# Optimization experiments

Measured on AMD Instinct MI355X. Metric: run time of the kernel, lower is better.

Reference implementation:

```python
import jax, jax.numpy as jnp
import numpy as np
import math

PSIZE = [(8, 8), (16, 16)]


def _conv2d(x, w, b):
    # 3x3 stride-1 'SAME' conv, NCHW / OIHW
    y = jax.lax.conv_general_dilated(
        x, w, window_strides=(1, 1), padding='SAME',
        dimension_numbers=('NCHW', 'OIHW', 'NCHW'))
    return y + b[None, :, None, None]


def _patch_attention(x, xs, b, t, c, h, w, ph, pw):
    oh, ow = h // ph, w // pw
    d = c * ph * pw
    # query: [b, oh*ow, c*ph*pw]
    q = x.reshape(b, c, oh, ph, ow, pw).transpose(0, 2, 4, 1, 3, 5).reshape(b, oh * ow, d)
    # key/value: [b, t*oh*ow, c*ph*pw]
    k = xs.reshape(b, t, c, oh, ph, ow, pw).transpose(0, 1, 3, 5, 2, 4, 6).reshape(b, t * oh * ow, d)
    scores = jnp.einsum('bqd,bkd->bqk', q, k) / jnp.asarray(math.sqrt(d), x.dtype)
    # NOTE: the original torch code calls scores.masked_fill(mm, -1e9) without
    # assigning the result, so the mask has NO effect; we faithfully omit it.
    atten = jax.nn.softmax(scores, axis=-1)
    val = jnp.einsum('bqk,bkd->bqd', atten, k)
    y = val.reshape(b, oh, ow, c, ph, pw).transpose(0, 3, 1, 4, 2, 5).reshape(b, c, h, w)
    return y


def setup_inputs() -> dict:
    key = jax.random.key(0)
    ks = jax.random.split(key, 6)
    b, t, c, h, w = 2, 5, 256, 128, 128
    n_p = len(PSIZE)
    x = jax.random.normal(ks[0], (b, c, h, w), dtype=jnp.float32)
    xs = jax.random.normal(ks[1], (b * t, c, h, w), dtype=jnp.float32)
    ms = jax.random.uniform(ks[2], (b * t, 1, h, w), dtype=jnp.float32)
    fan_lin = c * n_p * 9
    w_lin = jax.random.normal(ks[3], (c, c * n_p, 3, 3), dtype=jnp.float32) * (1.0 / math.sqrt(fan_lin))
    b_lin = jnp.zeros((c,), dtype=jnp.float32)
    fan_g = 512 * 9
    w_gate = jax.random.normal(ks[4], (c, 2 * c, 3, 3), dtype=jnp.float32) * (1.0 / math.sqrt(fan_g))
    b_gate = jnp.zeros((c,), dtype=jnp.float32)
    w_feat = jax.random.normal(ks[5], (c, 2 * c, 3, 3), dtype=jnp.float32) * (1.0 / math.sqrt(fan_g))
    b_feat = jnp.zeros((c,), dtype=jnp.float32)
    return {'x': x, 'xs': xs, 'ms': ms, 'w_lin': w_lin, 'b_lin': b_lin,
            'w_gate': w_gate, 'b_gate': b_gate, 'w_feat': w_feat, 'b_feat': b_feat}


def reference(x, xs, ms, w_lin, b_lin, w_gate, b_gate, w_feat, b_feat):
    b, c, h, w = x.shape
    t = xs.shape[0] // b
    outs = [_patch_attention(x, xs, b, t, c, h, w, ph, pw) for (ph, pw) in PSIZE]
    out = jnp.concatenate(outs, axis=1)                    # [b, c*len(psize), h, w]
    out = jax.nn.leaky_relu(_conv2d(out, w_lin, b_lin), 0.2)  # [b, c, h, w]
    fused = jnp.concatenate([x, out], axis=1)              # [b, 2c, h, w]
    gating = _conv2d(fused, w_gate, b_gate)
    feature = jax.nn.leaky_relu(_conv2d(fused, w_feat, b_feat), 0.2)
    x_out = jax.nn.sigmoid(gating) * feature               # [b, c, h, w]
    return x_out
```

## Files before the change

### kernel.cpp

```cpp
#include <hip/hip_runtime.h>

typedef unsigned short u16;
typedef unsigned int u32;
typedef __attribute__((ext_vector_type(8))) short bf16x8;
typedef __attribute__((ext_vector_type(4))) float f32x4;

#define MFMA16(d, a, bb) d = __builtin_amdgcn_mfma_f32_16x16x32_bf16(a, bb, d, 0, 0, 0)

#define PROW 130
#define PIMG 16900
#define PIMGC (16900 * 512)

__device__ __forceinline__ u16 f2bf(float f){
  union { float f; u32 i; } v; v.f = f;
  u32 r = v.i + 0x7fffu + ((v.i >> 16) & 1u);
  return (u16)(r >> 16);
}

__device__ __forceinline__ void gl16(const u16* g, u16* l){
  __builtin_amdgcn_global_load_lds(
      (const __attribute__((address_space(1))) u32*)g,
      (__attribute__((address_space(3))) u32*)l, 16, 0, 0);
}

__global__ __launch_bounds__(256) void k_border(u16* __restrict__ buf){
  const int b = blockIdx.y;
  const int j = blockIdx.x * 4 + (threadIdx.x >> 6);
  const int l = threadIdx.x & 63;
  int pp;
  if(j < 130)       pp = j;
  else if(j < 260)  pp = 129 * 130 + (j - 130);
  else if(j < 388)  pp = (j - 259) * 130;
  else              pp = (j - 387) * 130 + 129;
  u16* p = buf + ((size_t)b * PIMG + pp) * 512 + l * 8;
  *(uint4*)p = (uint4){0u, 0u, 0u, 0u};
}

__global__ __launch_bounds__(256) void k_transpose_pad(const float* __restrict__ in,
                                                       u16* __restrict__ out){
  __shared__ float s[32][33];
  const float* ip = in + (size_t)blockIdx.z * 256 * 16384;
  u16* op = out + (size_t)blockIdx.z * PIMGC;
  int r0 = blockIdx.x * 32, c0 = blockIdx.y * 32;
  int tx = threadIdx.x, ty = threadIdx.y;
#pragma unroll
  for(int i = 0; i < 4; ++i){
    int r = ty * 4 + i;
    s[r][tx] = ip[(size_t)(r0 + r) * 16384 + (c0 + tx)];
  }
  __syncthreads();
#pragma unroll
  for(int i = 0; i < 4; ++i){
    int pix = c0 + ty * 4 + i;
    u32 pp = ((u32)(pix >> 7) + 1) * PROW + (pix & 127) + 1;
    op[(size_t)pp * 512 + (r0 + tx)] = f2bf(s[tx][ty * 4 + i]);
  }
}

__global__ __launch_bounds__(256) void k_transpose(const float* __restrict__ in,
                                                   u16* __restrict__ out,
                                                   int rows, int cols,
                                                   int ostride, size_t o_imgstride){
  __shared__ float s[32][33];
  const float* ip = in + (size_t)blockIdx.z * (size_t)rows * (size_t)cols;
  u16* op = out + (size_t)blockIdx.z * o_imgstride;
  int r0 = blockIdx.x * 32, c0 = blockIdx.y * 32;
  int tx = threadIdx.x, ty = threadIdx.y;
#pragma unroll
  for(int i = 0; i < 4; ++i){
    int r = ty * 4 + i;
    s[r][tx] = ip[(size_t)(r0 + r) * cols + (c0 + tx)];
  }
  __syncthreads();
#pragma unroll
  for(int i = 0; i < 4; ++i){
    int c = ty * 4 + i;
    op[(size_t)(c0 + c) * ostride + (r0 + tx)] = f2bf(s[tx][c]);
  }
}

__global__ __launch_bounds__(256) void k_wt(const float* __restrict__ in,
                                            u16* __restrict__ out,
                                            int co_mul, int co_off, int co_tot){
  int ci = blockIdx.x * 256 + threadIdx.x;
  int co = blockIdx.y;
  int e  = blockIdx.z;
  out[((size_t)e * co_tot + co * co_mul + co_off) * 512 + ci] =
      f2bf(in[((size_t)co * 512 + ci) * 9 + e]);
}

__global__ __launch_bounds__(256) void k_scores8(const u16* __restrict__ FUSEDP,
                                                 const u16* __restrict__ XST,
                                                 float* __restrict__ S8p){
  __shared__ u16 As[4096], Bs[4096];
  const int bz = blockIdx.z, b = bz >> 3, g = bz & 7;
  const int q0 = blockIdx.x * 128, k0 = blockIdx.y * 128;
  const int tid = threadIdx.x, w = tid >> 6, l = tid & 63;
  const int wr = w >> 1, wc = w & 1;
  const int l15 = l & 15, kg = (l >> 4) * 8;
  f32x4 acc[4][4];
#pragma unroll
  for(int m = 0; m < 4; ++m)
#pragma unroll
    for(int n = 0; n < 4; ++n) acc[m][n] = (f32x4){0.f, 0.f, 0.f, 0.f};

  for(int e8 = 0; e8 < 8; ++e8){
    const int e = g * 8 + e8, dy = e >> 3, dx = e & 7;
    for(int ci0 = 0; ci0 < 256; ci0 += 32){
#pragma unroll
      for(int r = 0; r < 2; ++r){
        const int idx = (w * 2 + r) * 64 + l;
        const int q = q0 + (idx >> 2);
        const int apy = ((q >> 4) << 3) + dy, apx = ((q & 15) << 3) + dx;
        const size_t pa = ((size_t)b * PIMG + (size_t)(apy + 1) * PROW + apx + 1) * 512
                          + ci0 + (idx & 3) * 8;
        gl16(FUSEDP + pa, As + (size_t)(w * 2 + r) * 512);
        const int k = k0 + (idx >> 2), t = k >> 8, rm = k & 255;
        const size_t pb = (((size_t)b * 5 + t) * 16384 +
                           (size_t)(((rm >> 4) << 3) + dy) * 128 + ((rm & 15) << 3) + dx) * 256
                          + ci0 + (idx & 3) * 8;
        gl16(XST + pb, Bs + (size_t)(w * 2 + r) * 512);
      }
      __syncthreads();
      bf16x8 af[4], bq[4];
#pragma unroll
      for(int m = 0; m < 4; ++m) af[m] = *(const bf16x8*)(As + (wr * 64 + m * 16 + l15) * 32 + kg);
#pragma unroll
      for(int n = 0; n < 4; ++n) bq[n] = *(const bf16x8*)(Bs + (wc * 64 + n * 16 + l15) * 32 + kg);
#pragma unroll
      for(int m = 0; m < 4; ++m)
#pragma unroll
        for(int n = 0; n < 4; ++n)
          acc[m][n] = __builtin_amdgcn_mfma_f32_16x16x32_bf16(af[m], bq[n], acc[m][n], 0, 0, 0);
      __syncthreads();
    }
  }
  float* dst = S8p + ((size_t)g * 2 + b) * 256 * 1280;
#pragma unroll
  for(int m = 0; m < 4; ++m){
    const int q = q0 + wr * 64 + m * 16 + (l >> 4) * 4;
#pragma unroll
    for(int n = 0; n < 4; ++n){
      const int k = k0 + wc * 64 + n * 16 + l15;
#pragma unroll
      for(int r = 0; r < 4; ++r) dst[(size_t)(q + r) * 1280 + k] = acc[m][n][r];
    }
  }
}

__global__ __launch_bounds__(256) void k_softmax8(const float* __restrict__ S8p,
                                                  u16* __restrict__ A8){
  __shared__ float red[8];
  int b = blockIdx.x >> 8, q = blockIdx.x & 255;
  size_t roff = ((size_t)b * 256 + q) * 1280;
  int tid = threadIdx.x;
  float v[5]; float m = -1e30f;
#pragma unroll
  for(int i = 0; i < 5; ++i){
    size_t o = roff + tid + 256 * i;
    float s = 0.f;
#pragma unroll
    for(int g = 0; g < 8; ++g) s += S8p[(size_t)g * 655360 + o];
    v[i] = s * 0.0078125f; m = fmaxf(m, v[i]);
  }
#pragma unroll
  for(int o = 32; o > 0; o >>= 1) m = fmaxf(m, __shfl_xor(m, o));
  int wid = tid >> 6;
  if((tid & 63) == 0) red[wid] = m;
  __syncthreads();
  m = fmaxf(fmaxf(red[0], red[1]), fmaxf(red[2], red[3]));
  float s = 0.f;
#pragma unroll
  for(int i = 0; i < 5; ++i){ v[i] = __expf(v[i] - m); s += v[i]; }
#pragma unroll
  for(int o = 32; o > 0; o >>= 1) s += __shfl_xor(s, o);
  if((tid & 63) == 0) red[4 + wid] = s;
  __syncthreads();
  s = red[4] + red[5] + red[6] + red[7];
  float inv = 1.0f / s;
#pragma unroll
  for(int i = 0; i < 5; ++i) A8[roff + tid + 256 * i] = f2bf(v[i] * inv);
}

__global__ __launch_bounds__(320) void k_s16(const float* __restrict__ S8p,
                                             u16* __restrict__ A16){
  __shared__ float red[10];
  int b = blockIdx.x >> 6, q16 = blockIdx.x & 63;
  int tid = threadIdx.x;
  int t = tid >> 6, rm = tid & 63;
  int KY = rm >> 3, KX = rm & 7;
  int QY = q16 >> 3, QX = q16 & 7;
  float s = 0.f;
#pragma unroll
  for(int i = 0; i < 2; ++i)
#pragma unroll
    for(int j = 0; j < 2; ++j){
      int q8 = (2 * QY + i) * 16 + (2 * QX + j);
      int k8 = t * 256 + (2 * KY + i) * 16 + (2 * KX + j);
      size_t o = ((size_t)b * 256 + q8) * 1280 + k8;
#pragma unroll
      for(int g = 0; g < 8; ++g) s += S8p[(size_t)g * 655360 + o];
    }
  s *= 0.00390625f;
  float m = s;
#pragma unroll
  for(int o = 32; o > 0; o >>= 1) m = fmaxf(m, __shfl_xor(m, o));
  int wid = tid >> 6;
  if((tid & 63) == 0) red[wid] = m;
  __syncthreads();
  m = fmaxf(fmaxf(fmaxf(red[0], red[1]), fmaxf(red[2], red[3])), red[4]);
  float e = __expf(s - m);
  float sm = e;
#pragma unroll
  for(int o = 32; o > 0; o >>= 1) sm += __shfl_xor(sm, o);
  if((tid & 63) == 0) red[5 + wid] = sm;
  __syncthreads();
  sm = red[5] + red[6] + red[7] + red[8] + red[9];
  A16[((size_t)b * 64 + q16) * 320 + tid] = f2bf(e / sm);
}

__global__ __launch_bounds__(256) void k_val8(const u16* __restrict__ A8,
                                              const u16* __restrict__ XST,
                                              u16* __restrict__ OUTCATP){
  __shared__ u16 As[4096];
  __shared__ u16 Bs[128 * 40];
  const int z = blockIdx.z, b = z >> 6, rr = z & 63;
  const int ry = rr >> 3, rx = rr & 7;
  const int q0 = blockIdx.x * 128, c0 = blockIdx.y * 128;
  const int tid = threadIdx.x, w = tid >> 6, l = tid & 63;
  const int wr = w >> 1, wc = w & 1;
  const int l15 = l & 15, kg = (l >> 4) * 8;
  const int k2 = tid >> 4, ch8 = tid & 15;
  f32x4 acc[4][4];
#pragma unroll
  for(int m = 0; m < 4; ++m)
#pragma unroll
    for(int n = 0; n < 4; ++n) acc[m][n] = (f32x4){0.f, 0.f, 0.f, 0.f};

  for(int k0 = 0; k0 < 1280; k0 += 32){
#pragma unroll
    for(int r = 0; r < 2; ++r){
      const int idx = (w * 2 + r) * 64 + l;
      const u16* ga = A8 + ((size_t)b * 256 + q0 + (idx >> 2)) * 1280 + k0 + (idx & 3) * 8;
      gl16(ga, As + (size_t)(w * 2 + r) * 512);
    }
    {
      const int ka = k0 + k2 * 2, kb = ka + 1;
      const int ta = ka >> 8, ra = ka & 255;
      const int tb = kb >> 8, rb = kb & 255;
      const size_t pa = (((size_t)b * 5 + ta) * 16384 +
                         (size_t)(((ra >> 4) << 3) + ry) * 128 + ((ra & 15) << 3) + rx) * 256
                        + c0 + ch8 * 8;
      const size_t pb = (((size_t)b * 5 + tb) * 16384 +
                         (size_t)(((rb >> 4) << 3) + ry) * 128 + ((rb & 15) << 3) + rx) * 256
                        + c0 + ch8 * 8;
      union { uint4 v; u16 s[8]; } u0, u1;
      u0.v = *(const uint4*)(XST + pa);
      u1.v = *(const uint4*)(XST + pb);
      const int kloc = k2 * 2, swz = (ch8 & 3) << 3;
#pragma unroll
      for(int j = 0; j < 8; ++j){
        u32 pack = (u32)u0.s[j] | ((u32)u1.s[j] << 16);
        *(u32*)(Bs + (size_t)(ch8 * 8 + j) * 40 + (kloc ^ swz)) = pack;
      }
    }
    __syncthreads();
    bf16x8 af[4], bq[4];
#pragma unroll
    for(int m = 0; m < 4; ++m) af[m] = *(const bf16x8*)(As + (wr * 64 + m * 16 + l15) * 32 + kg);
#pragma unroll
    for(int n = 0; n < 4; ++n){
      const int ch = wc * 64 + n * 16 + l15;
      bq[n] = *(const bf16x8*)(Bs + (size_t)ch * 40 + (kg ^ (((ch >> 3) & 3) << 3)));
    }
#pragma unroll
    for(int m = 0; m < 4; ++m)
#pragma unroll
      for(int n = 0; n < 4; ++n)
        acc[m][n] = __builtin_amdgcn_mfma_f32_16x16x32_bf16(af[m], bq[n], acc[m][n], 0, 0, 0);
    __syncthreads();
  }
#pragma unroll
  for(int m = 0; m < 4; ++m){
    const int qb = q0 + wr * 64 + m * 16 + (l >> 4) * 4;
#pragma unroll
    for(int n = 0; n < 4; ++n){
      const int ch = c0 + wc * 64 + n * 16 + l15;
#pragma unroll
      for(int r = 0; r < 4; ++r){
        const int q = qb + r;
        const int py = ((q >> 4) << 3) + ry, px = ((q & 15) << 3) + rx;
        OUTCATP[((size_t)b * PIMG + (size_t)(py + 1) * PROW + px + 1) * 512 + ch] = f2bf(acc[m][n][r]);
      }
    }
  }
}

__global__ __launch_bounds__(256) void k_val16(const u16* __restrict__ A16,
                                               const u16* __restrict__ XST,
                                               u16* __restrict__ OUTCATP){
  __shared__ u16 As[64 * 32];
  __shared__ u16 Bs[128 * 40];
  const int z = blockIdx.z, b = z >> 8, rr = z & 255;
  const int ry = rr >> 4, rx = rr & 15;
  const int c0 = blockIdx.y * 128;
  const int tid = threadIdx.x, w = tid >> 6, l = tid & 63;
  const int l15 = l & 15, kg = (l >> 4) * 8;
  const int k2 = tid >> 4, ch8 = tid & 15;
  f32x4 acc[4][2];
#pragma unroll
  for(int m = 0; m < 4; ++m)
#pragma unroll
    for(int n = 0; n < 2; ++n) acc[m][n] = (f32x4){0.f, 0.f, 0.f, 0.f};

  for(int k0 = 0; k0 < 320; k0 += 32){
    {
      const int idx = w * 64 + l;
      const u16* ga = A16 + ((size_t)b * 64 + (idx >> 2)) * 320 + k0 + (idx & 3) * 8;
      gl16(ga, As + (size_t)w * 512);
    }
    {
      const int ka = k0 + k2 * 2, kb = ka + 1;
      const int ta = ka >> 6, ra = ka & 63;
      const int tb = kb >> 6, rb = kb & 63;
      const size_t pa = (((size_t)b * 5 + ta) * 16384 +
                         (size_t)(((ra >> 3) << 4) + ry) * 128 + ((ra & 7) << 4) + rx) * 256
                        + c0 + ch8 * 8;
      const size_t pb = (((size_t)b * 5 + tb) * 16384 +
                         (size_t)(((rb >> 3) << 4) + ry) * 128 + ((rb & 7) << 4) + rx) * 256
                        + c0 + ch8 * 8;
      union { uint4 v; u16 s[8]; } u0, u1;
      u0.v = *(const uint4*)(XST + pa);
      u1.v = *(const uint4*)(XST + pb);
      const int kloc = k2 * 2, swz = (ch8 & 3) << 3;
#pragma unroll
      for(int j = 0; j < 8; ++j){
        u32 pack = (u32)u0.s[j] | ((u32)u1.s[j] << 16);
        *(u32*)(Bs + (size_t)(ch8 * 8 + j) * 40 + (kloc ^ swz)) = pack;
      }
    }
    __syncthreads();
    bf16x8 af[4], bq[2];
#pragma unroll
    for(int m = 0; m < 4; ++m) af[m] = *(const bf16x8*)(As + (m * 16 + l15) * 32 + kg);
#pragma unroll
    for(int n = 0; n < 2; ++n){
      const int ch = w * 32 + n * 16 + l15;
      bq[n] = *(const bf16x8*)(Bs + (size_t)ch * 40 + (kg ^ (((ch >> 3) & 3) << 3)));
    }
#pragma unroll
    for(int m = 0; m < 4; ++m)
#pragma unroll
      for(int n = 0; n < 2; ++n)
        acc[m][n] = __builtin_amdgcn_mfma_f32_16x16x32_bf16(af[m], bq[n], acc[m][n], 0, 0, 0);
    __syncthreads();
  }
#pragma unroll
  for(int m = 0; m < 4; ++m){
    const int qb = m * 16 + (l >> 4) * 4;
#pragma unroll
    for(int n = 0; n < 2; ++n){
      const int ch = c0 + w * 32 + n * 16 + l15;
#pragma unroll
      for(int r = 0; r < 4; ++r){
        const int q = qb + r;
        const int py = ((q >> 3) << 4) + ry, px = ((q & 7) << 4) + rx;
        OUTCATP[((size_t)b * PIMG + (size_t)(py + 1) * PROW + px + 1) * 512 + 256 + ch] = f2bf(acc[m][n][r]);
      }
    }
  }
}

__global__ __launch_bounds__(512, 4) void k_convA(const u16* __restrict__ A,
                                                  const u16* __restrict__ W,
                                                  const float* __restrict__ bias,
                                                  u16* __restrict__ FUSEDP){
  constexpr int NT = 72;
  __shared__ u16 lds[2][16384];
  const int id = blockIdx.x;
  const int wg = (id & 7) * 64 + (id >> 3);
  const int mt = wg & 127, rest = wg >> 7;
  const int n0 = (rest & 1) * 128, b = rest >> 1;
  const int m0 = mt * 128;
  const int tid = threadIdx.x, w = tid >> 6, l = tid & 63;
  const int wr = w >> 2, wc = w & 3;
  const int l15 = l & 15, lq = l >> 4;
  const int lr = l >> 3;
  const u32 laneswz = (u32)((((l & 7) * 16) ^ (lr << 4)) >> 1);

  u32 aB[2], bB[2];
#pragma unroll
  for(int j = 0; j < 2; ++j){
    const int row = (w * 2 + j) * 8 + lr;
    const int p = m0 + row;
    aB[j] = ((u32)b * PIMG + ((u32)(p >> 7) + 1) * PROW + (u32)(p & 127) + 1) * 512 + laneswz;
    bB[j] = (u32)(n0 + row) * 512 + laneswz;
  }

  f32x4 acc[4][2];
#pragma unroll
  for(int m = 0; m < 4; ++m)
#pragma unroll
    for(int n = 0; n < 2; ++n) acc[m][n] = (f32x4){0.f, 0.f, 0.f, 0.f};

  auto STAGE = [&](int kt){
    const int e = kt % 9, ci0 = (kt / 9) << 6;
    const int dy = e / 3 - 1, dx = e % 3 - 1;
    const int aD = (dy * PROW + dx) * 512 + ci0;
    const u32 bD = (u32)e * 256u * 512u + ci0;
    u16* bufA = &lds[kt & 1][0];
    u16* bufB = &lds[kt & 1][8192];
#pragma unroll
    for(int j = 0; j < 2; ++j){
      const int c = w * 2 + j;
      gl16(A + aB[j] + aD, bufA + c * 512);
      gl16(W + bB[j] + bD, bufB + c * 512);
    }
  };

  STAGE(0);
  STAGE(1);

  for(int t = 0; t < NT; ++t){
    if(t < NT - 1) asm volatile("s_waitcnt vmcnt(4)" ::: "memory");
    else           asm volatile("s_waitcnt vmcnt(0)" ::: "memory");
    __builtin_amdgcn_s_barrier();
    const char* bufA = (const char*)&lds[t & 1][0];
    const char* bufB = bufA + 16384;
    bf16x8 af[4][2], bq[2][2];
#pragma unroll
    for(int m = 0; m < 4; ++m){
      const int row = wr * 64 + m * 16 + l15;
      const int sz = (row & 7) << 4;
#pragma unroll
      for(int kk = 0; kk < 2; ++kk)
        af[m][kk] = *(const bf16x8*)(bufA + row * 128 + (((kk * 4 + lq) * 16) ^ sz));
    }
#pragma unroll
    for(int n = 0; n < 2; ++n){
      const int row = wc * 32 + n * 16 + l15;
      const int sz = (row & 7) << 4;
#pragma unroll
      for(int kk = 0; kk < 2; ++kk)
        bq[n][kk] = *(const bf16x8*)(bufB + row * 128 + (((kk * 4 + lq) * 16) ^ sz));
    }
    asm volatile("s_waitcnt lgkmcnt(0)" ::: "memory");
    __builtin_amdgcn_sched_barrier(0);
    __builtin_amdgcn_s_barrier();
    if(t + 2 < NT) STAGE(t + 2);
    __builtin_amdgcn_s_setprio(1);
#pragma unroll
    for(int kk = 0; kk < 2; ++kk)
#pragma unroll
      for(int m = 0; m < 4; ++m)
#pragma unroll
        for(int n = 0; n < 2; ++n)
          MFMA16(acc[m][n], af[m][kk], bq[n][kk]);
    __builtin_amdgcn_s_setprio(0);
  }

#pragma unroll
  for(int m = 0; m < 4; ++m){
    const int p0 = m0 + wr * 64 + m * 16 + lq * 4;
    const size_t pp = ((size_t)b * PIMG + (size_t)((p0 >> 7) + 1) * PROW + (p0 & 127) + 1) * 512;
#pragma unroll
    for(int n = 0; n < 2; ++n){
      const int co = n0 + wc * 32 + n * 16 + l15;
      const float bi = bias[co];
#pragma unroll
      for(int r = 0; r < 4; ++r){
        float v = acc[m][n][r] + bi;
        v = v > 0.f ? v : 0.2f * v;
        FUSEDP[pp + (size_t)r * 512 + 256 + co] = f2bf(v);
      }
    }
  }
}

__global__ __launch_bounds__(1024, 4) void k_convB16(const u16* __restrict__ A,
                                                     const u16* __restrict__ W,
                                                     const float* __restrict__ bias,
                                                     const float* __restrict__ bias2,
                                                     float* __restrict__ out){
  constexpr int NT = 72;
  __shared__ u16 lds[2][32768];
  const int id = blockIdx.x;
  const int wg = (id & 7) * 32 + (id >> 3);
  const int ntile = wg >> 7;
  const int rem = wg & 127, b = rem >> 6, mt = rem & 63;
  const int m0 = mt * 256, n0 = ntile * 256;
  const int tid = threadIdx.x, w = tid >> 6, l = tid & 63;
  const int wr = w >> 2, wc = w & 3;
  const int l15 = l & 15, lq = l >> 4;
  const int lr = l >> 3;
  const u32 laneswz = (u32)((((l & 7) * 16) ^ (lr << 4)) >> 1);

  u32 aB[2], bB[2];
#pragma unroll
  for(int j = 0; j < 2; ++j){
    const int row = (w * 2 + j) * 8 + lr;
    const int p = m0 + row;
    aB[j] = ((u32)b * PIMG + ((u32)(p >> 7) + 1) * PROW + (u32)(p & 127) + 1) * 512 + laneswz;
    bB[j] = (u32)(n0 + row) * 512 + laneswz;
  }

  f32x4 acc[4][4];
#pragma unroll
  for(int m = 0; m < 4; ++m)
#pragma unroll
    for(int n = 0; n < 4; ++n) acc[m][n] = (f32x4){0.f, 0.f, 0.f, 0.f};

  auto STAGE = [&](int kt){
    const int e = kt % 9, ci0 = (kt / 9) << 6;
    const int dy = e / 3 - 1, dx = e % 3 - 1;
    const int aD = (dy * PROW + dx) * 512 + ci0;
    const u32 bD = (u32)e * 512u * 512u + ci0;
    u16* bufA = &lds[kt & 1][0];
    u16* bufB = &lds[kt & 1][16384];
#pragma unroll
    for(int j = 0; j < 2; ++j){
      const int c = w * 2 + j;
      gl16(A + aB[j] + aD, bufA + c * 512);
      gl16(W + bB[j] + bD, bufB + c * 512);
    }
  };

  STAGE(0);
  STAGE(1);

  for(int t = 0; t < NT; ++t){
    if(t < NT - 1) asm volatile("s_waitcnt vmcnt(4)" ::: "memory");
    else           asm volatile("s_waitcnt vmcnt(0)" ::: "memory");
    __builtin_amdgcn_s_barrier();
    const char* bufA = (const char*)&lds[t & 1][0];
    const char* bufB = bufA + 32768;
    bf16x8 af[4], bq[4];
#pragma unroll
    for(int m = 0; m < 4; ++m){
      const int row = wr * 64 + m * 16 + l15;
      af[m] = *(const bf16x8*)(bufA + row * 128 + ((lq * 16) ^ ((row & 7) << 4)));
    }
#pragma unroll
    for(int n = 0; n < 4; ++n){
      const int row = wc * 64 + n * 16 + l15;
      bq[n] = *(const bf16x8*)(bufB + row * 128 + ((lq * 16) ^ ((row & 7) << 4)));
    }
    asm volatile("s_waitcnt lgkmcnt(0)" ::: "memory");
    __builtin_amdgcn_sched_barrier(0);
    __builtin_amdgcn_s_setprio(1);
#pragma unroll
    for(int m = 0; m < 4; ++m)
#pragma unroll
      for(int n = 0; n < 4; ++n)
        MFMA16(acc[m][n], af[m], bq[n]);
    __builtin_amdgcn_s_setprio(0);
#pragma unroll
    for(int m = 0; m < 4; ++m){
      const int row = wr * 64 + m * 16 + l15;
      af[m] = *(const bf16x8*)(bufA + row * 128 + ((64 + lq * 16) ^ ((row & 7) << 4)));
    }
#pragma unroll
    for(int n = 0; n < 4; ++n){
      const int row = wc * 64 + n * 16 + l15;
      bq[n] = *(const bf16x8*)(bufB + row * 128 + ((64 + lq * 16) ^ ((row & 7) << 4)));
    }
    asm volatile("s_waitcnt lgkmcnt(0)" ::: "memory");
    __builtin_amdgcn_sched_barrier(0);
    __builtin_amdgcn_s_barrier();
    if(t + 2 < NT) STAGE(t + 2);
    __builtin_amdgcn_s_setprio(1);
#pragma unroll
    for(int m = 0; m < 4; ++m)
#pragma unroll
      for(int n = 0; n < 4; ++n)
        MFMA16(acc[m][n], af[m], bq[n]);
    __builtin_amdgcn_s_setprio(0);
  }

#pragma unroll
  for(int m = 0; m < 4; ++m){
    const int p0 = m0 + wr * 64 + m * 16 + lq * 4;
#pragma unroll
    for(int n = 0; n < 4; ++n){
      const int col = n0 + wc * 64 + n * 16 + l15;
      const int s = col & 1, co = col >> 1;
      const float big = bias[co], bif = bias2[co];
      float res[4];
#pragma unroll
      for(int r = 0; r < 4; ++r){
        const float val = acc[m][n][r];
        const float oth = __shfl_xor(val, 1);
        float gg = s ? oth : val;
        float ff = s ? val : oth;
        gg += big; ff += bif;
        ff = ff > 0.f ? ff : 0.2f * ff;
        res[r] = ff / (1.0f + __expf(-gg));
      }
      if(s == 0){
        float4 v4 = make_float4(res[0], res[1], res[2], res[3]);
        *(float4*)&out[((size_t)b * 256 + co) * 16384 + p0] = v4;
      }
    }
  }
}

extern "C" void kernel_launch(void* const* d_in, const int* in_sizes, int n_in,
                              void* d_out, int out_size, void* d_ws, size_t ws_size,
                              hipStream_t stream){
  const float* x      = (const float*)d_in[0];
  const float* xs     = (const float*)d_in[1];
  const float* w_lin  = (const float*)d_in[3];
  const float* b_lin  = (const float*)d_in[4];
  const float* w_gate = (const float*)d_in[5];
  const float* b_gate = (const float*)d_in[6];
  const float* w_feat = (const float*)d_in[7];
  const float* b_feat = (const float*)d_in[8];
  float* out = (float*)d_out;

  char* ws = (char*)d_ws;
  size_t off = 0;
  auto alloc = [&](size_t bytes) -> void* {
    void* p = ws + off;
    off += (bytes + 255) & ~(size_t)255;
    return p;
  };
  u16* FUSEDP  = (u16*)alloc(2ull * PIMGC * 2);
  u16* OUTCATP = (u16*)alloc(2ull * PIMGC * 2);
  u16* XST     = (u16*)alloc(10ull * 16384 * 256 * 2);
  u16* WTl     = (u16*)alloc(9ull * 256 * 512 * 2);
  u16* WGF     = (u16*)alloc(9ull * 512 * 512 * 2);
  float* S8p   = (float*)alloc(8ull * 655360 * 4);
  u16* A8      = (u16*)alloc(655360ull * 2);
  u16* A16     = (u16*)alloc(2ull * 64 * 320 * 2);

  k_border<<<dim3(129, 2), 256, 0, stream>>>(FUSEDP);
  k_border<<<dim3(129, 2), 256, 0, stream>>>(OUTCATP);

  dim3 tb(32, 8);
  k_transpose_pad<<<dim3(8, 512, 2), tb, 0, stream>>>(x, FUSEDP);
  k_transpose<<<dim3(8, 512, 10), tb, 0, stream>>>(xs, XST, 256, 16384, 256, 4194304ull);

  k_wt<<<dim3(2, 256, 9), 256, 0, stream>>>(w_lin,  WTl, 1, 0, 256);
  k_wt<<<dim3(2, 256, 9), 256, 0, stream>>>(w_gate, WGF, 2, 0, 512);
  k_wt<<<dim3(2, 256, 9), 256, 0, stream>>>(w_feat, WGF, 2, 1, 512);

  k_scores8<<<dim3(2, 10, 16), 256, 0, stream>>>(FUSEDP, XST, S8p);
  k_softmax8<<<512, 256, 0, stream>>>(S8p, A8);
  k_s16<<<128, 320, 0, stream>>>(S8p, A16);

  k_val8 <<<dim3(2, 2, 128), 256, 0, stream>>>(A8, XST, OUTCATP);
  k_val16<<<dim3(1, 2, 512), 256, 0, stream>>>(A16, XST, OUTCATP);

  k_convA<<<512, 512, 0, stream>>>(OUTCATP, WTl, b_lin, FUSEDP);
  k_convB16<<<256, 1024, 0, stream>>>(FUSEDP, WGF, b_gate, b_feat, out);
}
```

Before: 405.2 us.

## Vectorize transposes, coalesce weight reorder, double-buffer swizzled scores8 GEMM

Transpose kernels now handle 64-channel tiles and emit 16-byte packed bf16 stores instead of scalar u16 writes. Weight reordering reads each input's 9 taps contiguously in one thread rather than striding. The 8x8 score GEMM moves to 512 threads with double-buffered LDS, 64-wide K steps, an XOR-swizzled LDS layout, explicit waitcnt/barrier pipelining and raised MFMA priority, all aimed at hiding global-load latency and avoiding LDS bank conflicts. This adds fragile hand-written vmcnt counts and much more LDS per block.

```diff
diff --git a/kernel.cpp b/kernel.cpp
--- a/kernel.cpp
+++ b/kernel.cpp
@@ -36,112 +36,159 @@
   *(uint4*)p = (uint4){0u, 0u, 0u, 0u};
 }
 
-__global__ __launch_bounds__(256) void k_transpose_pad(const float* __restrict__ in,
-                                                       u16* __restrict__ out){
-  __shared__ float s[32][33];
+__global__ __launch_bounds__(256) void k_transPadW(const float* __restrict__ in,
+                                                   u16* __restrict__ out){
+  __shared__ float s[64][33];
   const float* ip = in + (size_t)blockIdx.z * 256 * 16384;
   u16* op = out + (size_t)blockIdx.z * PIMGC;
-  int r0 = blockIdx.x * 32, c0 = blockIdx.y * 32;
-  int tx = threadIdx.x, ty = threadIdx.y;
-#pragma unroll
-  for(int i = 0; i < 4; ++i){
-    int r = ty * 4 + i;
+  const int r0 = blockIdx.x * 64, c0 = blockIdx.y * 32;
+  const int tx = threadIdx.x, ty = threadIdx.y;
+#pragma unroll
+  for(int i = 0; i < 8; ++i){
+    int r = ty * 8 + i;
     s[r][tx] = ip[(size_t)(r0 + r) * 16384 + (c0 + tx)];
   }
   __syncthreads();
-#pragma unroll
-  for(int i = 0; i < 4; ++i){
-    int pix = c0 + ty * 4 + i;
-    u32 pp = ((u32)(pix >> 7) + 1) * PROW + (pix & 127) + 1;
-    op[(size_t)pp * 512 + (r0 + tx)] = f2bf(s[tx][ty * 4 + i]);
-  }
-}
-
-__global__ __launch_bounds__(256) void k_transpose(const float* __restrict__ in,
-                                                   u16* __restrict__ out,
-                                                   int rows, int cols,
-                                                   int ostride, size_t o_imgstride){
-  __shared__ float s[32][33];
-  const float* ip = in + (size_t)blockIdx.z * (size_t)rows * (size_t)cols;
+  const int tid = ty * 32 + tx;
+  const int p = tid >> 3, cs = (tid & 7) * 8;
+  const int pix = c0 + p;
+  const u32 pp = ((u32)(pix >> 7) + 1) * PROW + (pix & 127) + 1;
+  union { uint4 v; u16 h[8]; } pk;
+#pragma unroll
+  for(int i = 0; i < 8; ++i) pk.h[i] = f2bf(s[cs + i][p]);
+  *(uint4*)(op + (size_t)pp * 512 + r0 + cs) = pk.v;
+}
+
+__global__ __launch_bounds__(256) void k_transW(const float* __restrict__ in,
+                                                u16* __restrict__ out,
+                                                int cols, int ostride,
+                                                size_t o_imgstride){
+  __shared__ float s[64][33];
+  const float* ip = in + (size_t)blockIdx.z * 256 * (size_t)cols;
   u16* op = out + (size_t)blockIdx.z * o_imgstride;
-  int r0 = blockIdx.x * 32, c0 = blockIdx.y * 32;
-  int tx = threadIdx.x, ty = threadIdx.y;
-#pragma unroll
-  for(int i = 0; i < 4; ++i){
-    int r = ty * 4 + i;
+  const int r0 = blockIdx.x * 64, c0 = blockIdx.y * 32;
+  const int tx = threadIdx.x, ty = threadIdx.y;
+#pragma unroll
+  for(int i = 0; i < 8; ++i){
+    int r = ty * 8 + i;
     s[r][tx] = ip[(size_t)(r0 + r) * cols + (c0 + tx)];
   }
   __syncthreads();
-#pragma unroll
-  for(int i = 0; i < 4; ++i){
-    int c = ty * 4 + i;
-    op[(size_t)(c0 + c) * ostride + (r0 + tx)] = f2bf(s[tx][c]);
-  }
-}
-
-__global__ __launch_bounds__(256) void k_wt(const float* __restrict__ in,
-                                            u16* __restrict__ out,
-                                            int co_mul, int co_off, int co_tot){
-  int ci = blockIdx.x * 256 + threadIdx.x;
-  int co = blockIdx.y;
-  int e  = blockIdx.z;
-  out[((size_t)e * co_tot + co * co_mul + co_off) * 512 + ci] =
-      f2bf(in[((size_t)co * 512 + ci) * 9 + e]);
-}
-
-__global__ __launch_bounds__(256) void k_scores8(const u16* __restrict__ FUSEDP,
-                                                 const u16* __restrict__ XST,
-                                                 float* __restrict__ S8p){
-  __shared__ u16 As[4096], Bs[4096];
+  const int tid = ty * 32 + tx;
+  const int p = tid >> 3, cs = (tid & 7) * 8;
+  union { uint4 v; u16 h[8]; } pk;
+#pragma unroll
+  for(int i = 0; i < 8; ++i) pk.h[i] = f2bf(s[cs + i][p]);
+  *(uint4*)(op + (size_t)(c0 + p) * ostride + r0 + cs) = pk.v;
+}
+
+__global__ __launch_bounds__(512) void k_wt2(const float* __restrict__ in,
+                                             u16* __restrict__ out,
+                                             int co_mul, int co_off, int co_tot){
+  const int ci = threadIdx.x;
+  const int co = blockIdx.x;
+  const float* src = in + ((size_t)co * 512 + ci) * 9;
+  float v[9];
+#pragma unroll
+  for(int e = 0; e < 9; ++e) v[e] = src[e];
+#pragma unroll
+  for(int e = 0; e < 9; ++e)
+    out[((size_t)e * co_tot + co * co_mul + co_off) * 512 + ci] = f2bf(v[e]);
+}
+
+__global__ __launch_bounds__(512, 4) void k_scores8(const u16* __restrict__ FUSEDP,
+                                                    const u16* __restrict__ XST,
+                                                    float* __restrict__ S8p){
+  constexpr int NT = 32;
+  __shared__ u16 lds[2][16384];
   const int bz = blockIdx.z, b = bz >> 3, g = bz & 7;
   const int q0 = blockIdx.x * 128, k0 = blockIdx.y * 128;
   const int tid = threadIdx.x, w = tid >> 6, l = tid & 63;
-  const int wr = w >> 1, wc = w & 1;
-  const int l15 = l & 15, kg = (l >> 4) * 8;
-  f32x4 acc[4][4];
+  const int wr = w >> 2, wc = w & 3;
+  const int l15 = l & 15, lq = l >> 4;
+  const int lr = l >> 3, lc = l & 7;
+  const u32 laneswz = (u32)(((lc * 16) ^ (lr << 4)) >> 1);
+
+  u32 aB[2], bB[2];
+#pragma unroll
+  for(int j = 0; j < 2; ++j){
+    const int row = (w * 2 + j) * 8 + lr;
+    const int q = q0 + row, qy = q >> 4, qx = q & 15;
+    const u32 pp = (u32)(qy * 8 + g + 1) * PROW + qx * 8 + 1;
+    aB[j] = ((u32)b * PIMG + pp) * 512 + laneswz;
+    const int k = k0 + row, t = k >> 8, rm = k & 255;
+    const u32 bpix = (u32)((rm >> 4) * 8 + g) * 128 + (rm & 15) * 8;
+    bB[j] = (((u32)b * 5 + t) * 16384 + bpix) * 256 + laneswz;
+  }
+
+  f32x4 acc[4][2];
 #pragma unroll
   for(int m = 0; m < 4; ++m)
 #pragma unroll
-    for(int n = 0; n < 4; ++n) acc[m][n] = (f32x4){0.f, 0.f, 0.f, 0.f};
-
-  for(int e8 = 0; e8 < 8; ++e8){
-    const int e = g * 8 + e8, dy = e >> 3, dx = e & 7;
-    for(int ci0 = 0; ci0 < 256; ci0 += 32){
-#pragma unroll
-      for(int r = 0; r < 2; ++r){
-        const int idx = (w * 2 + r) * 64 + l;
-        const int q = q0 + (idx >> 2);
-        const int apy = ((q >> 4) << 3) + dy, apx = ((q & 15) << 3) + dx;
-        const size_t pa = ((size_t)b * PIMG + (size_t)(apy + 1) * PROW + apx + 1) * 512
-                          + ci0 + (idx & 3) * 8;
-        gl16(FUSEDP + pa, As + (size_t)(w * 2 + r) * 512);
-        const int k = k0 + (idx >> 2), t = k >> 8, rm = k & 255;
-        const size_t pb = (((size_t)b * 5 + t) * 16384 +
-                           (size_t)(((rm >> 4) << 3) + dy) * 128 + ((rm & 15) << 3) + dx) * 256
-                          + ci0 + (idx & 3) * 8;
-        gl16(XST + pb, Bs + (size_t)(w * 2 + r) * 512);
-      }
-      __syncthreads();
-      bf16x8 af[4], bq[4];
-#pragma unroll
-      for(int m = 0; m < 4; ++m) af[m] = *(const bf16x8*)(As + (wr * 64 + m * 16 + l15) * 32 + kg);
-#pragma unroll
-      for(int n = 0; n < 4; ++n) bq[n] = *(const bf16x8*)(Bs + (wc * 64 + n * 16 + l15) * 32 + kg);
+    for(int n = 0; n < 2; ++n) acc[m][n] = (f32x4){0.f, 0.f, 0.f, 0.f};
+
+  auto STAGE = [&](int kt){
+    const int e8 = kt & 7, ci0 = (kt >> 3) << 6;
+    const int aD = e8 * 512 + ci0;
+    const int bD = e8 * 256 + ci0;
+    u16* bufA = &lds[kt & 1][0];
+    u16* bufB = &lds[kt & 1][8192];
+#pragma unroll
+    for(int j = 0; j < 2; ++j){
+      const int c = w * 2 + j;
+      gl16(FUSEDP + aB[j] + aD, bufA + c * 512);
+      gl16(XST + bB[j] + bD, bufB + c * 512);
+    }
+  };
+
+  STAGE(0);
+  STAGE(1);
+
+  for(int t = 0; t < NT; ++t){
+    if(t < NT - 1) asm volatile("s_waitcnt vmcnt(4)" ::: "memory");
+    else           asm volatile("s_waitcnt vmcnt(0)" ::: "memory");
+    __builtin_amdgcn_s_barrier();
+    const char* bufA = (const char*)&lds[t & 1][0];
+    const char* bufB = bufA + 16384;
+    bf16x8 af[4][2], bq[2][2];
+#pragma unroll
+    for(int m = 0; m < 4; ++m){
+      const int row = wr * 64 + m * 16 + l15;
+      const int sz = (row & 7) << 4;
+#pragma unroll
+      for(int kk = 0; kk < 2; ++kk)
+        af[m][kk] = *(const bf16x8*)(bufA + row * 128 + (((kk * 4 + lq) * 16) ^ sz));
+    }
+#pragma unroll
+    for(int n = 0; n < 2; ++n){
+      const int row = wc * 32 + n * 16 + l15;
+      const int sz = (row & 7) << 4;
+#pragma unroll
+      for(int kk = 0; kk < 2; ++kk)
+        bq[n][kk] = *(const bf16x8*)(bufB + row * 128 + (((kk * 4 + lq) * 16) ^ sz));
+    }
+    asm volatile("s_waitcnt lgkmcnt(0)" ::: "memory");
+    __builtin_amdgcn_sched_barrier(0);
+    __builtin_amdgcn_s_barrier();
+    if(t + 2 < NT) STAGE(t + 2);
+    __builtin_amdgcn_s_setprio(1);
+#pragma unroll
+    for(int kk = 0; kk < 2; ++kk)
 #pragma unroll
       for(int m = 0; m < 4; ++m)
 #pragma unroll
-        for(int n = 0; n < 4; ++n)
-          acc[m][n] = __builtin_amdgcn_mfma_f32_16x16x32_bf16(af[m], bq[n], acc[m][n], 0, 0, 0);
-      __syncthreads();
-    }
-  }
+        for(int n = 0; n < 2; ++n)
+          MFMA16(acc[m][n], af[m][kk], bq[n][kk]);
+    __builtin_amdgcn_s_setprio(0);
+  }
+
   float* dst = S8p + ((size_t)g * 2 + b) * 256 * 1280;
 #pragma unroll
   for(int m = 0; m < 4; ++m){
-    const int q = q0 + wr * 64 + m * 16 + (l >> 4) * 4;
-#pragma unroll
-    for(int n = 0; n < 4; ++n){
-      const int k = k0 + wc * 64 + n * 16 + l15;
+    const int q = q0 + wr * 64 + m * 16 + lq * 4;
+#pragma unroll
+    for(int n = 0; n < 2; ++n){
+      const int k = k0 + wc * 32 + n * 16 + l15;
 #pragma unroll
       for(int r = 0; r < 4; ++r) dst[(size_t)(q + r) * 1280 + k] = acc[m][n][r];
     }
@@ -637,14 +684,14 @@
   k_border<<<dim3(129, 2), 256, 0, stream>>>(OUTCATP);
 
   dim3 tb(32, 8);
-  k_transpose_pad<<<dim3(8, 512, 2), tb, 0, stream>>>(x, FUSEDP);
-  k_transpose<<<dim3(8, 512, 10), tb, 0, stream>>>(xs, XST, 256, 16384, 256, 4194304ull);
-
-  k_wt<<<dim3(2, 256, 9), 256, 0, stream>>>(w_lin,  WTl, 1, 0, 256);
-  k_wt<<<dim3(2, 256, 9), 256, 0, stream>>>(w_gate, WGF, 2, 0, 512);
-  k_wt<<<dim3(2, 256, 9), 256, 0, stream>>>(w_feat, WGF, 2, 1, 512);
-
-  k_scores8<<<dim3(2, 10, 16), 256, 0, stream>>>(FUSEDP, XST, S8p);
+  k_transPadW<<<dim3(4, 512, 2), tb, 0, stream>>>(x, FUSEDP);
+  k_transW<<<dim3(4, 512, 10), tb, 0, stream>>>(xs, XST, 16384, 256, 4194304ull);
+
+  k_wt2<<<256, 512, 0, stream>>>(w_lin,  WTl, 1, 0, 256);
+  k_wt2<<<256, 512, 0, stream>>>(w_gate, WGF, 2, 0, 512);
+  k_wt2<<<256, 512, 0, stream>>>(w_feat, WGF, 2, 1, 512);
+
+  k_scores8<<<dim3(2, 10, 16), 512, 0, stream>>>(FUSEDP, XST, S8p);
   k_softmax8<<<512, 256, 0, stream>>>(S8p, A8);
   k_s16<<<128, 320, 0, stream>>>(S8p, A16);
 
```

Measured after the change: 391.7 us. 3.3% less time.
